# Kernel optimization log

Hardware: AMD Instinct MI355X
Metric: run time of the kernel (lower is better)

The kernel has to match this reference:

```python
import jax, jax.numpy as jnp
import numpy as np

N, P, E = 100000, 10000, 500000
DN, DP, DK, SKIP, MLP_H = 256, 128, 100, 27, 64
E_MEAN, E_STD = 4.0, 2.0
ETA_MEAN, ETA_STD = 0.0, 1.5
ATT_NORM = 0.1  # 1/sqrt(100)
LN_EPS, RMS_EPS = 1e-5, 1e-6


def setup_inputs() -> dict:
    key = jax.random.key(0)
    ks = jax.random.split(key, 32)
    DIN = DN + SKIP  # 283
    s = 0.05
    inp = {
        'node_hidden': jax.random.normal(ks[0], (N, DN), jnp.float32),
        'energy': jax.random.uniform(ks[1], (N,), jnp.float32, 0.01, 1.0),
        'eta': jax.random.normal(ks[2], (N,), jnp.float32),
        'phi': jax.random.normal(ks[3], (N,), jnp.float32),
        'layer': jax.random.uniform(ks[4], (N,), jnp.float32),
        'eta_l': jax.random.normal(ks[5], (N, 6), jnp.float32),
        'phi_l': jax.random.normal(ks[6], (N, 6), jnp.float32),
        'ene_l': jax.random.normal(ks[7], (N, 6), jnp.float32),
        'track_feats': jax.random.uniform(ks[8], (N, 5), jnp.float32),
        'particle_hidden': jax.random.normal(ks[9], (P, DP), jnp.float32),
        'global_rep': jax.random.normal(ks[10], (P, DN), jnp.float32),
        'edge_src': jax.random.randint(ks[11], (E,), 0, N, jnp.int32),
        'edge_dst': jax.random.randint(ks[12], (E,), 0, P, jnp.int32),
        # learned params
        'W_key': jax.random.normal(ks[13], (DIN, DK), jnp.float32) * s,
        'b_key': jnp.zeros((DK,), jnp.float32),
        'W_val': jax.random.normal(ks[14], (DIN, DP), jnp.float32) * s,
        'b_val': jnp.zeros((DP,), jnp.float32),
        'W_q': jax.random.normal(ks[15], (DP + DN, DK), jnp.float32) * s,
        'b_q': jnp.zeros((DK,), jnp.float32),
        'W_ih': jax.random.normal(ks[16], (DP, 3 * DP), jnp.float32) * s,
        'b_ih': jnp.zeros((3 * DP,), jnp.float32),
        'W_hh': jax.random.normal(ks[17], (DP, 3 * DP), jnp.float32) * s,
        'b_hh': jnp.zeros((3 * DP,), jnp.float32),
        'ln_g': jnp.ones((DP,), jnp.float32),
        'ln_b': jnp.zeros((DP,), jnp.float32),
        'W1': jax.random.normal(ks[18], (DP, MLP_H), jnp.float32) * s,
        'b1': jnp.zeros((MLP_H,), jnp.float32),
        'W2': jax.random.normal(ks[19], (MLP_H, DP), jnp.float32) * s,
        'b2': jnp.zeros((DP,), jnp.float32),
        'rms_w': jnp.ones((DP,), jnp.float32),
        'lin_w': jax.random.normal(ks[20], (1, DP), jnp.float32),
    }
    return inp


def _forward(node_hidden, energy, eta, phi, layer, eta_l, phi_l, ene_l, track_feats,
             particle_hidden, global_rep,
             W_key, b_key, W_val, b_val, W_q, b_q, W_ih, b_ih, W_hh, b_hh,
             ln_g, ln_b, W1, b1, W2, b2, rms_w, lin_w, edge_src, edge_dst):
    # --- build node inputs: hidden rep + 27 skip scalars (same order as torch cat) ---
    skip = jnp.concatenate([
        ((jnp.log(energy) - E_MEAN) / E_STD)[:, None],
        ((eta - ETA_MEAN) / ETA_STD)[:, None],
        phi[:, None], layer[:, None],
        (eta_l - ETA_MEAN) / ETA_STD,  # eta_l1..l6
        phi_l, ene_l,
        track_feats,  # isTrack, nTracks, tracks_pt, nTracks_4, tracks_pt_4
    ], axis=1)  # [N, 27]
    x = jnp.concatenate([node_hidden, skip], axis=1)  # [N, 283]
    keys = x @ W_key + b_key      # [N, 100]
    vals = x @ W_val + b_val      # [N, DP]
    q = jnp.concatenate([particle_hidden, global_rep], axis=1) @ W_q + b_q  # [P, 100]

    # --- per-edge attention (note: node_update consumes RAW relu attention) ---
    att = jax.nn.relu(jnp.sum(keys[edge_src] * q[edge_dst], axis=1) * ATT_NORM)  # [E]
    msg = att[:, None] * vals[edge_src]                                          # [E, DP]
    ws = jax.ops.segment_sum(msg, edge_dst, num_segments=P)                      # [P, DP]

    # --- node update: rmsnorm * sigmoid(eltwise) gating, GRU, LN, MLP residual ---
    rms = ws * jax.lax.rsqrt(jnp.mean(ws * ws, axis=-1, keepdims=True) + RMS_EPS) * rms_w
    gated = rms * jax.nn.sigmoid(ws * lin_w)

    h = particle_hidden
    gi = gated @ W_ih + b_ih
    gh = h @ W_hh + b_hh
    i_r, i_z, i_n = jnp.split(gi, 3, axis=1)
    h_r, h_z, h_n = jnp.split(gh, 3, axis=1)
    r = jax.nn.sigmoid(i_r + h_r)
    z = jax.nn.sigmoid(i_z + h_z)
    n = jnp.tanh(i_n + r * h_n)
    h_new = (1.0 - z) * n + z * h

    mu = jnp.mean(h_new, axis=-1, keepdims=True)
    var = jnp.mean((h_new - mu) ** 2, axis=-1, keepdims=True)
    ln = (h_new - mu) * jax.lax.rsqrt(var + LN_EPS) * ln_g + ln_b
    mlp = jax.nn.relu(ln @ W1 + b1) @ W2 + b2
    return h + mlp  # updated particle 'node hidden rep'


def reference(node_hidden, energy, eta, phi, layer, eta_l, phi_l, ene_l, track_feats,
              particle_hidden, global_rep, edge_src, edge_dst,
              W_key, b_key, W_val, b_val, W_q, b_q, W_ih, b_ih, W_hh, b_hh,
              ln_g, ln_b, W1, b1, W2, b2, rms_w, lin_w):
    return _forward(node_hidden, energy, eta, phi, layer, eta_l, phi_l, ene_l, track_feats,
                    particle_hidden, global_rep,
                    W_key, b_key, W_val, b_val, W_q, b_q, W_ih, b_ih, W_hh, b_hh,
                    ln_g, ln_b, W1, b1, W2, b2, rms_w, lin_w, edge_src, edge_dst)
```

## Files before the change

kernel.cpp:

```cpp
#include <hip/hip_runtime.h>
#include <hip/hip_bf16.h>
#include <math.h>

#define THREADS 256

typedef __bf16 bf16_t;
typedef __bf16 bf16x8 __attribute__((ext_vector_type(8)));
typedef float f32x4 __attribute__((ext_vector_type(4)));

__device__ __forceinline__ float sigmoidf_(float x) { return 1.f / (1.f + expf(-x)); }

__device__ __forceinline__ void gload_lds16(const void* g, void* l) {
    __builtin_amdgcn_global_load_lds((const __attribute__((address_space(1))) void*)g,
                                     (__attribute__((address_space(3))) void*)l, 16, 0, 0);
}

__device__ __forceinline__ bf16x8 cvt8(float4 a, float4 b) {
    bf16x8 v;
    v[0] = (bf16_t)a.x; v[1] = (bf16_t)a.y; v[2] = (bf16_t)a.z; v[3] = (bf16_t)a.w;
    v[4] = (bf16_t)b.x; v[5] = (bf16_t)b.y; v[6] = (bf16_t)b.z; v[7] = (bf16_t)b.w;
    return v;
}

__global__ void prep_kernel(const float* __restrict__ W_key, const float* __restrict__ W_val,
                            const float* __restrict__ W_q, const float* __restrict__ b_key,
                            const float* __restrict__ b_val, const float* __restrict__ b_q,
                            bf16_t* __restrict__ WbfT, bf16_t* __restrict__ WqT,
                            float* __restrict__ bpn, float* __restrict__ bpq)
{
    int i = blockIdx.x * THREADS + threadIdx.x;
    const int NW = 256 * 288, NQ = 128 * 384;
    if (i < NW) {
        int c = i / 288, k = i - c * 288;
        float v = 0.f;
        if (k < 283) {
            if (c < 100) v = W_key[k * 100 + c];
            else if (c >= 128 && c < 256) v = W_val[k * 128 + (c - 128)];
        }
        WbfT[i] = (bf16_t)v;
    } else if (i < NW + NQ) {
        int j = i - NW;
        int c = j / 384, k = j - c * 384;
        WqT[j] = (bf16_t)((c < 100) ? W_q[k * 100 + c] : 0.f);
    } else if (i < NW + NQ + 256) {
        int c = i - NW - NQ;
        bpn[c] = (c < 100) ? b_key[c] : ((c >= 128 && c < 256) ? b_val[c - 128] : 0.f);
    } else if (i < NW + NQ + 256 + 128) {
        int c = i - NW - NQ - 256;
        bpq[c] = (c < 100) ? b_q[c] : 0.f;
    }
}

__global__ void prep2_kernel(const float* __restrict__ W_ih, const float* __restrict__ W_hh,
                             const float* __restrict__ b_ih, const float* __restrict__ b_hh,
                             const float* __restrict__ W1, const float* __restrict__ b1,
                             const float* __restrict__ W2,
                             bf16_t* __restrict__ BTg, bf16_t* __restrict__ W1Tp,
                             bf16_t* __restrict__ W2Tp, float* __restrict__ bgru,
                             float* __restrict__ b1p,
                             int* __restrict__ cnt, int twoP,
                             bf16_t* __restrict__ AG, int padStart, int padElems)
{
    int i = blockIdx.x * THREADS + threadIdx.x;
    const int NG = 768 * 256, N1 = 128 * 128, N2 = 128 * 128;
    const int NB = NG + N1 + N2 + 768 + 128;
    if (i < NG) {
        int c = i >> 8, k = i & 255;
        float v = 0.f;
        if (c < 384) { if (k < 128) v = W_ih[k * 384 + c]; }
        else         { if (k >= 128) v = W_hh[(k - 128) * 384 + (c - 384)]; }
        BTg[i] = (bf16_t)v;
    } else if (i < NG + N1) {
        int j = i - NG; int c = j >> 7, k = j & 127;
        W1Tp[j] = (bf16_t)((c < 64) ? W1[k * 64 + c] : 0.f);
    } else if (i < NG + N1 + N2) {
        int j = i - NG - N1; int c = j >> 7, k = j & 127;
        W2Tp[j] = (bf16_t)((k < 64) ? W2[k * 128 + c] : 0.f);
    } else if (i < NG + N1 + N2 + 768) {
        int c = i - NG - N1 - N2;
        bgru[c] = (c < 384) ? b_ih[c] : b_hh[c - 384];
    } else if (i < NB) {
        int c = i - NG - N1 - N2 - 768;
        b1p[c] = (c < 64) ? b1[c] : 0.f;
    } else if (i < NB + twoP) {
        cnt[i - NB] = 0;
    } else if (i < NB + twoP + padElems) {
        int j = i - NB - twoP;
        AG[(size_t)padStart * 256 + j] = (bf16_t)0.f;
    }
}

__global__ void skip_kernel(const float* __restrict__ energy, const float* __restrict__ eta,
                            const float* __restrict__ phi, const float* __restrict__ layer,
                            const float* __restrict__ eta_l, const float* __restrict__ phi_l,
                            const float* __restrict__ ene_l, const float* __restrict__ track,
                            bf16_t* __restrict__ skipb, int N_, int Mpad)
{
    int n = blockIdx.x * THREADS + threadIdx.x;
    if (n >= Mpad) return;
    float o[32];
#pragma unroll
    for (int j = 0; j < 32; ++j) o[j] = 0.f;
    if (n < N_) {
        o[0] = (logf(energy[n]) - 4.0f) * 0.5f;
        o[1] = eta[n] * (1.f / 1.5f);
        o[2] = phi[n];
        o[3] = layer[n];
#pragma unroll
        for (int j = 0; j < 6; ++j) o[4 + j]  = eta_l[n * 6 + j] * (1.f / 1.5f);
#pragma unroll
        for (int j = 0; j < 6; ++j) o[10 + j] = phi_l[n * 6 + j];
#pragma unroll
        for (int j = 0; j < 6; ++j) o[16 + j] = ene_l[n * 6 + j];
#pragma unroll
        for (int j = 0; j < 5; ++j) o[22 + j] = track[n * 5 + j];
    }
    bf16_t* dst = skipb + (size_t)n * 32;
#pragma unroll
    for (int g = 0; g < 4; ++g) {
        bf16x8 v;
#pragma unroll
        for (int j = 0; j < 8; ++j) v[j] = (bf16_t)o[g * 8 + j];
        *(bf16x8*)(dst + g * 8) = v;
    }
}

__global__ __launch_bounds__(256) void kv_gemm(
    const float* __restrict__ nh, const bf16_t* __restrict__ skipb,
    const bf16_t* __restrict__ BT, const float* __restrict__ bias,
    bf16_t* __restrict__ KVb, int N_)
{
    int tid = threadIdx.x;
    int w = tid >> 6, lane = tid & 63;
    int la = lane & 15, hi = lane >> 4;
    int row0 = blockIdx.x * 32;
    int col0 = w * 64;
    int r0 = row0 + la, r1 = row0 + 16 + la;
    bool ok0 = r0 < N_, ok1 = r1 < N_;
    const float* pa0 = nh + (size_t)r0 * 256 + hi * 8;
    const float* pa1 = nh + (size_t)r1 * 256 + hi * 8;

    f32x4 zero4 = {0.f, 0.f, 0.f, 0.f};
    f32x4 acc[2][4];
#pragma unroll
    for (int i = 0; i < 2; ++i)
#pragma unroll
        for (int j = 0; j < 4; ++j) acc[i][j] = zero4;

    for (int kt = 0; kt < 288; kt += 32) {
        bf16x8 a0, a1;
        if (kt < 256) {
            bf16x8 z = {};
            a0 = ok0 ? cvt8(*(const float4*)(pa0 + kt), *(const float4*)(pa0 + kt + 4)) : z;
            a1 = ok1 ? cvt8(*(const float4*)(pa1 + kt), *(const float4*)(pa1 + kt + 4)) : z;
        } else {
            a0 = *(const bf16x8*)(skipb + (size_t)r0 * 32 + hi * 8);
            a1 = *(const bf16x8*)(skipb + (size_t)r1 * 32 + hi * 8);
        }
        bf16x8 b[4];
#pragma unroll
        for (int j = 0; j < 4; ++j)
            b[j] = *(const bf16x8*)(BT + (size_t)(col0 + j * 16 + la) * 288 + kt + hi * 8);
#pragma unroll
        for (int j = 0; j < 4; ++j) {
            acc[0][j] = __builtin_amdgcn_mfma_f32_16x16x32_bf16(a0, b[j], acc[0][j], 0, 0, 0);
            acc[1][j] = __builtin_amdgcn_mfma_f32_16x16x32_bf16(a1, b[j], acc[1][j], 0, 0, 0);
        }
    }

#pragma unroll
    for (int j = 0; j < 4; ++j) {
        int col = col0 + j * 16 + la;
        float bb = bias[col];
#pragma unroll
        for (int i = 0; i < 2; ++i) {
#pragma unroll
            for (int r = 0; r < 4; ++r) {
                int row = row0 + i * 16 + hi * 4 + r;
                KVb[(size_t)row * 256 + col] = (bf16_t)(acc[i][j][r] + bb);
            }
        }
    }
}

template <int MODE>
__global__ __launch_bounds__(256) void mfma_gemm(
    const void* __restrict__ A0, const void* __restrict__ A1,
    const bf16_t* __restrict__ BT, const float* __restrict__ bias,
    void* __restrict__ out0v, const float* __restrict__ resid,
    int K, int Mlimit, int Nrows)
{
    __shared__ short AsS[64 * 32];
    __shared__ short BsS[128 * 32];
    int tid = threadIdx.x;
    int lane = tid & 63, w = tid >> 6;
    int la = lane & 15, hi = lane >> 4;
    int m0 = (w & 1) * 32, n0 = (w >> 1) * 64;
    int row0 = blockIdx.y * 64, col0 = blockIdx.x * 128;

    f32x4 zero4 = {0.f, 0.f, 0.f, 0.f};
    f32x4 acc[2][4];
#pragma unroll
    for (int i = 0; i < 2; ++i)
#pragma unroll
        for (int j = 0; j < 4; ++j) acc[i][j] = zero4;

    const int ra = tid >> 2, ka = (tid & 3) * 8;
    const int c1 = tid + 256;
    const int rb0 = tid >> 2, kb0 = (tid & 3) * 8;
    const int rb1 = c1 >> 2,  kb1 = (c1 & 3) * 8;

    for (int kt = 0; kt < K; kt += 32) {
        int gmA = row0 + ra;
        if (MODE == 1) {
            int gk = kt + ka;
            bf16x8 v = {};
            if (gmA < Nrows) {
                const float* s = (gk < 128) ? ((const float*)A0 + (size_t)gmA * 128 + gk)
                                            : ((const float*)A1 + (size_t)gmA * 256 + (gk - 128));
                v = cvt8(*(const float4*)s, *(const float4*)(s + 4));
            }
            *(bf16x8*)(AsS + (size_t)tid * 8) = v;
        } else {
            gload_lds16((const bf16_t*)A0 + (size_t)gmA * K + kt + ka,
                        AsS + (size_t)tid * 8);
        }
        gload_lds16(BT + (size_t)(col0 + rb0) * K + kt + kb0, BsS + (size_t)tid * 8);
        gload_lds16(BT + (size_t)(col0 + rb1) * K + kt + kb1, BsS + (size_t)c1 * 8);
        __syncthreads();
        bf16x8 a[2], b[4];
#pragma unroll
        for (int i = 0; i < 2; ++i)
            a[i] = *(const bf16x8*)(AsS + (m0 + i * 16 + la) * 32 + hi * 8);
#pragma unroll
        for (int j = 0; j < 4; ++j)
            b[j] = *(const bf16x8*)(BsS + (n0 + j * 16 + la) * 32 + hi * 8);
#pragma unroll
        for (int i = 0; i < 2; ++i)
#pragma unroll
            for (int j = 0; j < 4; ++j)
                acc[i][j] = __builtin_amdgcn_mfma_f32_16x16x32_bf16(a[i], b[j], acc[i][j], 0, 0, 0);
        __syncthreads();
    }

#pragma unroll
    for (int i = 0; i < 2; ++i) {
#pragma unroll
        for (int j = 0; j < 4; ++j) {
            int col = col0 + n0 + j * 16 + la;
            float bb = bias[col];
#pragma unroll
            for (int r = 0; r < 4; ++r) {
                int row = row0 + m0 + i * 16 + hi * 4 + r;
                float v = acc[i][j][r] + bb;
                if (MODE == 1) {
                    ((bf16_t*)out0v)[(size_t)row * 128 + col] = (bf16_t)v;
                } else if (MODE == 2) {
                    ((float*)out0v)[(size_t)row * 768 + col] = v;
                } else if (MODE == 3) {
                    ((bf16_t*)out0v)[(size_t)row * 128 + col] = (bf16_t)fmaxf(v, 0.f);
                } else {
                    if (row < Mlimit)
                        ((float*)out0v)[(size_t)row * 128 + col] = v + resid[(size_t)row * 128 + col];
                }
            }
        }
    }
}

__global__ void hist_kernel(const int* __restrict__ dst, int* __restrict__ cnt, int E_)
{
    int i = blockIdx.x * THREADS + threadIdx.x;
    if (i < E_) atomicAdd(&cnt[dst[i]], 1);
}

__global__ void scan_kernel(const int* __restrict__ cnt, int* __restrict__ offb, int P_)
{
    __shared__ int wsum[16];
    int tid = threadIdx.x;
    int lane = tid & 63, w = tid >> 6;
    int base = tid * 10;
    int c[10];
    int s = 0;
#pragma unroll
    for (int j = 0; j < 10; ++j) {
        int i = base + j;
        c[j] = (i < P_) ? cnt[i] : 0;
        s += c[j];
    }
    int pre = s;
    for (int o = 1; o < 64; o <<= 1) {
        int t = __shfl_up(pre, o);
        if (lane >= o) pre += t;
    }
    if (lane == 63) wsum[w] = pre;
    __syncthreads();
    if (w == 0 && lane < 16) {
        int v = wsum[lane];
        for (int o = 1; o < 16; o <<= 1) {
            int t = __shfl_up(v, o, 16);
            if (lane >= o) v += t;
        }
        wsum[lane] = v;
    }
    __syncthreads();
    int waveoff = (w == 0) ? 0 : wsum[w - 1];
    int run = waveoff + pre - s;
#pragma unroll
    for (int j = 0; j < 10; ++j) {
        int i = base + j;
        if (i <= P_) offb[i] = run;
        run += c[j];
    }
}

__global__ void fill_src_kernel(const int* __restrict__ dst, const int* __restrict__ src,
                                const int* __restrict__ offb, int* __restrict__ cur,
                                int* __restrict__ csrc, int E_)
{
    int i = blockIdx.x * THREADS + threadIdx.x;
    if (i < E_) {
        int d = dst[i];
        int pos = atomicAdd(&cur[d], 1);
        csrc[offb[d] + pos] = src[i];
    }
}

__global__ __launch_bounds__(256) void edge_kernel(
    const int* __restrict__ offb, const int* __restrict__ csrc,
    const bf16_t* __restrict__ KVb, const bf16_t* __restrict__ Qb,
    const float* __restrict__ ph, const float* __restrict__ rms_w,
    const float* __restrict__ lin_w, bf16_t* __restrict__ AG, int P_)
{
    int tid = threadIdx.x;
    int p = blockIdx.x * 4 + (tid >> 6);
    if (p >= P_) return;
    int lane = tid & 63;
    int c = lane & 15, g = lane >> 4;

    bf16x8 q8 = *(const bf16x8*)(Qb + (size_t)p * 128 + c * 8);
    float qf[8];
#pragma unroll
    for (int j = 0; j < 8; ++j) qf[j] = (float)q8[j];

    int s0 = offb[p], e0 = offb[p + 1];
    float acc[8] = {};

    int i = s0 + g;
    for (; i + 12 < e0; i += 16) {
        int n0 = csrc[i], n1 = csrc[i + 4], n2 = csrc[i + 8], n3 = csrc[i + 12];
        const bf16_t* b0 = KVb + (size_t)n0 * 256 + c * 8;
        const bf16_t* b1 = KVb + (size_t)n1 * 256 + c * 8;
        const bf16_t* b2 = KVb + (size_t)n2 * 256 + c * 8;
        const bf16_t* b3 = KVb + (size_t)n3 * 256 + c * 8;
        bf16x8 k0 = *(const bf16x8*)b0, v0 = *(const bf16x8*)(b0 + 128);
        bf16x8 k1 = *(const bf16x8*)b1, v1 = *(const bf16x8*)(b1 + 128);
        bf16x8 k2 = *(const bf16x8*)b2, v2 = *(const bf16x8*)(b2 + 128);
        bf16x8 k3 = *(const bf16x8*)b3, v3 = *(const bf16x8*)(b3 + 128);
        float d0 = 0.f, d1 = 0.f, d2 = 0.f, d3 = 0.f;
#pragma unroll
        for (int j = 0; j < 8; ++j) {
            d0 += qf[j] * (float)k0[j]; d1 += qf[j] * (float)k1[j];
            d2 += qf[j] * (float)k2[j]; d3 += qf[j] * (float)k3[j];
        }
        d0 += __shfl_xor(d0, 1); d1 += __shfl_xor(d1, 1); d2 += __shfl_xor(d2, 1); d3 += __shfl_xor(d3, 1);
        d0 += __shfl_xor(d0, 2); d1 += __shfl_xor(d1, 2); d2 += __shfl_xor(d2, 2); d3 += __shfl_xor(d3, 2);
        d0 += __shfl_xor(d0, 4); d1 += __shfl_xor(d1, 4); d2 += __shfl_xor(d2, 4); d3 += __shfl_xor(d3, 4);
        d0 += __shfl_xor(d0, 8); d1 += __shfl_xor(d1, 8); d2 += __shfl_xor(d2, 8); d3 += __shfl_xor(d3, 8);
        float a0 = fmaxf(d0 * 0.1f, 0.f), a1 = fmaxf(d1 * 0.1f, 0.f);
        float a2 = fmaxf(d2 * 0.1f, 0.f), a3 = fmaxf(d3 * 0.1f, 0.f);
#pragma unroll
        for (int j = 0; j < 8; ++j)
            acc[j] += a0 * (float)v0[j] + a1 * (float)v1[j]
                    + a2 * (float)v2[j] + a3 * (float)v3[j];
    }
    for (; i < e0; i += 4) {
        int nA = csrc[i];
        const bf16_t* bA = KVb + (size_t)nA * 256 + c * 8;
        bf16x8 kA = *(const bf16x8*)bA;
        bf16x8 vA = *(const bf16x8*)(bA + 128);
        float dA = 0.f;
#pragma unroll
        for (int j = 0; j < 8; ++j) dA += qf[j] * (float)kA[j];
        dA += __shfl_xor(dA, 1);
        dA += __shfl_xor(dA, 2);
        dA += __shfl_xor(dA, 4);
        dA += __shfl_xor(dA, 8);
        float aA = fmaxf(dA * 0.1f, 0.f);
#pragma unroll
        for (int j = 0; j < 8; ++j) acc[j] += aA * (float)vA[j];
    }

#pragma unroll
    for (int j = 0; j < 8; ++j) {
        acc[j] += __shfl_xor(acc[j], 16);
        acc[j] += __shfl_xor(acc[j], 32);
    }

    float ss = 0.f;
#pragma unroll
    for (int j = 0; j < 8; ++j) ss += acc[j] * acc[j];
    ss += __shfl_xor(ss, 1); ss += __shfl_xor(ss, 2); ss += __shfl_xor(ss, 4); ss += __shfl_xor(ss, 8);
    float scale = rsqrtf(ss * (1.f / 128.f) + 1e-6f);
    if (g == 0) {
        int cb = c * 8;
        const float* hp = ph + (size_t)p * 128 + cb;
        float4 ha = *(const float4*)hp, hb = *(const float4*)(hp + 4);
        float hv[8] = {ha.x, ha.y, ha.z, ha.w, hb.x, hb.y, hb.z, hb.w};
        bf16x8 gv, hvb;
#pragma unroll
        for (int j = 0; j < 8; ++j) {
            float wsv = acc[j];
            float rv = wsv * scale * rms_w[cb + j];
            gv[j] = (bf16_t)(rv * sigmoidf_(wsv * lin_w[cb + j]));
            hvb[j] = (bf16_t)hv[j];
        }
        *(bf16x8*)(AG + (size_t)p * 256 + cb) = gv;
        *(bf16x8*)(AG + (size_t)p * 256 + 128 + cb) = hvb;
    }
}

__global__ void gru_ln_kernel(const float* __restrict__ G768, const float* __restrict__ ph,
                              const float* __restrict__ ln_g, const float* __restrict__ ln_b,
                              bf16_t* __restrict__ LNb, int P_, int Mq)
{
    int tid = threadIdx.x;
    int g = tid >> 4, s = tid & 15;
    int p = blockIdx.x * 16 + g;
    if (p >= Mq) return;
    int cb = s * 8;
    if (p >= P_) {
        bf16x8 z = {};
        *(bf16x8*)(LNb + (size_t)p * 128 + cb) = z;
        return;
    }
    const float* G = G768 + (size_t)p * 768;
    float ir[8], iz[8], in_[8], hr[8], hz[8], hn_[8], hv[8];
#pragma unroll
    for (int q = 0; q < 2; ++q) {
        float4 v;
        v = *(const float4*)(G + cb + q * 4);        ir[q*4]=v.x; ir[q*4+1]=v.y; ir[q*4+2]=v.z; ir[q*4+3]=v.w;
        v = *(const float4*)(G + 128 + cb + q * 4);  iz[q*4]=v.x; iz[q*4+1]=v.y; iz[q*4+2]=v.z; iz[q*4+3]=v.w;
        v = *(const float4*)(G + 256 + cb + q * 4);  in_[q*4]=v.x; in_[q*4+1]=v.y; in_[q*4+2]=v.z; in_[q*4+3]=v.w;
        v = *(const float4*)(G + 384 + cb + q * 4);  hr[q*4]=v.x; hr[q*4+1]=v.y; hr[q*4+2]=v.z; hr[q*4+3]=v.w;
        v = *(const float4*)(G + 512 + cb + q * 4);  hz[q*4]=v.x; hz[q*4+1]=v.y; hz[q*4+2]=v.z; hz[q*4+3]=v.w;
        v = *(const float4*)(G + 640 + cb + q * 4);  hn_[q*4]=v.x; hn_[q*4+1]=v.y; hn_[q*4+2]=v.z; hn_[q*4+3]=v.w;
        v = *(const float4*)(ph + (size_t)p * 128 + cb + q * 4);
        hv[q*4]=v.x; hv[q*4+1]=v.y; hv[q*4+2]=v.z; hv[q*4+3]=v.w;
    }
    float hn[8];
    float sm = 0.f, sq = 0.f;
#pragma unroll
    for (int j = 0; j < 8; ++j) {
        float r = sigmoidf_(ir[j] + hr[j]);
        float z = sigmoidf_(iz[j] + hz[j]);
        float n = tanhf(in_[j] + r * hn_[j]);
        hn[j] = (1.f - z) * n + z * hv[j];
        sm += hn[j]; sq += hn[j] * hn[j];
    }
    sm += __shfl_xor(sm, 1); sm += __shfl_xor(sm, 2); sm += __shfl_xor(sm, 4); sm += __shfl_xor(sm, 8);
    sq += __shfl_xor(sq, 1); sq += __shfl_xor(sq, 2); sq += __shfl_xor(sq, 4); sq += __shfl_xor(sq, 8);
    float mu = sm * (1.f / 128.f);
    float var = sq * (1.f / 128.f) - mu * mu;
    float iv = rsqrtf(var + 1e-5f);
    bf16x8 o;
#pragma unroll
    for (int j = 0; j < 8; ++j) {
        int c = cb + j;
        o[j] = (bf16_t)((hn[j] - mu) * iv * ln_g[c] + ln_b[c]);
    }
    *(bf16x8*)(LNb + (size_t)p * 128 + cb) = o;
}

extern "C" void kernel_launch(void* const* d_in, const int* in_sizes, int n_in,
                              void* d_out, int out_size, void* d_ws, size_t ws_size,
                              hipStream_t stream)
{
    const float* nh      = (const float*)d_in[0];
    const float* energy  = (const float*)d_in[1];
    const float* eta     = (const float*)d_in[2];
    const float* phi     = (const float*)d_in[3];
    const float* layer   = (const float*)d_in[4];
    const float* eta_l   = (const float*)d_in[5];
    const float* phi_l   = (const float*)d_in[6];
    const float* ene_l   = (const float*)d_in[7];
    const float* track   = (const float*)d_in[8];
    const float* ph      = (const float*)d_in[9];
    const float* grep    = (const float*)d_in[10];
    const int*   esrc    = (const int*)d_in[11];
    const int*   edst    = (const int*)d_in[12];
    const float* W_key   = (const float*)d_in[13];
    const float* b_key   = (const float*)d_in[14];
    const float* W_val   = (const float*)d_in[15];
    const float* b_val   = (const float*)d_in[16];
    const float* W_q     = (const float*)d_in[17];
    const float* b_q     = (const float*)d_in[18];
    const float* W_ih    = (const float*)d_in[19];
    const float* b_ih    = (const float*)d_in[20];
    const float* W_hh    = (const float*)d_in[21];
    const float* b_hh    = (const float*)d_in[22];
    const float* ln_g    = (const float*)d_in[23];
    const float* ln_b    = (const float*)d_in[24];
    const float* W1      = (const float*)d_in[25];
    const float* b1      = (const float*)d_in[26];
    const float* W2      = (const float*)d_in[27];
    const float* b2      = (const float*)d_in[28];
    const float* rms_w   = (const float*)d_in[29];
    const float* lin_w   = (const float*)d_in[30];

    const int N = in_sizes[1];
    const int P = in_sizes[9] / 128;
    const int E = in_sizes[11];
    const int Mpad = ((N + 127) / 128) * 128;
    const int Mq   = ((P + 127) / 128) * 128;

    char* base = (char*)d_ws;
    size_t off = 0;
    auto alloc = [&](size_t bytes) { void* p = base + off; off = (off + bytes + 255) & ~(size_t)255; return p; };
    bf16_t* skipb = (bf16_t*)alloc((size_t)Mpad * 32 * 2);
    bf16_t* WbfT  = (bf16_t*)alloc(256 * 288 * 2);
    bf16_t* WqT   = (bf16_t*)alloc(128 * 384 * 2);
    float*  bpn   = (float*)alloc(256 * 4);
    float*  bpq   = (float*)alloc(128 * 4);
    bf16_t* KVb   = (bf16_t*)alloc((size_t)Mpad * 256 * 2);
    bf16_t* Qb    = (bf16_t*)alloc((size_t)Mq * 128 * 2);
    int*    cnt   = (int*)alloc((size_t)(2 * P) * 4);
    int*    cur   = cnt + P;
    int*    offb  = (int*)alloc((size_t)(P + 1) * 4);
    int*    csrc  = (int*)alloc((size_t)E * 4);
    bf16_t* AG    = (bf16_t*)alloc((size_t)Mq * 256 * 2);
    bf16_t* BTg   = (bf16_t*)alloc(768 * 256 * 2);
    bf16_t* W1Tp  = (bf16_t*)alloc(128 * 128 * 2);
    bf16_t* W2Tp  = (bf16_t*)alloc(128 * 128 * 2);
    float*  bgru  = (float*)alloc(768 * 4);
    float*  b1p   = (float*)alloc(128 * 4);
    float*  G768  = (float*)alloc((size_t)Mq * 768 * 4);
    bf16_t* LNb   = (bf16_t*)alloc((size_t)Mq * 128 * 2);
    bf16_t* M1    = (bf16_t*)alloc((size_t)Mq * 128 * 2);

    {
        int total = 256 * 288 + 128 * 384 + 256 + 128;
        prep_kernel<<<(total + THREADS - 1) / THREADS, THREADS, 0, stream>>>(
            W_key, W_val, W_q, b_key, b_val, b_q, WbfT, WqT, bpn, bpq);
        int padElems = (Mq - P) * 256;
        int total2 = 768 * 256 + 128 * 128 + 128 * 128 + 768 + 128 + 2 * P + padElems;
        prep2_kernel<<<(total2 + THREADS - 1) / THREADS, THREADS, 0, stream>>>(
            W_ih, W_hh, b_ih, b_hh, W1, b1, W2, BTg, W1Tp, W2Tp, bgru, b1p,
            cnt, 2 * P, AG, P, padElems);
        skip_kernel<<<(Mpad + THREADS - 1) / THREADS, THREADS, 0, stream>>>(
            energy, eta, phi, layer, eta_l, phi_l, ene_l, track, skipb, N, Mpad);
    }
    kv_gemm<<<Mpad / 32, THREADS, 0, stream>>>(nh, skipb, WbfT, bpn, KVb, N);
    mfma_gemm<1><<<dim3(1, Mq / 64), THREADS, 0, stream>>>(
        ph, grep, WqT, bpq, Qb, nullptr, 384, 0, P);
    hist_kernel<<<(E + THREADS - 1) / THREADS, THREADS, 0, stream>>>(edst, cnt, E);
    scan_kernel<<<1, 1024, 0, stream>>>(cnt, offb, P);
    fill_src_kernel<<<(E + THREADS - 1) / THREADS, THREADS, 0, stream>>>(
        edst, esrc, offb, cur, csrc, E);
    edge_kernel<<<(P + 3) / 4, THREADS, 0, stream>>>(
        offb, csrc, KVb, Qb, ph, rms_w, lin_w, AG, P);
    mfma_gemm<2><<<dim3(6, Mq / 64), THREADS, 0, stream>>>(
        AG, nullptr, BTg, bgru, G768, nullptr, 256, 0, Mq);
    gru_ln_kernel<<<Mq / 16, THREADS, 0, stream>>>(G768, ph, ln_g, ln_b, LNb, P, Mq);
    mfma_gemm<3><<<dim3(1, Mq / 64), THREADS, 0, stream>>>(
        LNb, nullptr, W1Tp, b1p, M1, nullptr, 128, 0, Mq);
    mfma_gemm<4><<<dim3(1, Mq / 64), THREADS, 0, stream>>>(
        M1, nullptr, W2Tp, b2, d_out, ph, 128, P, Mq);
}
```

Measured before the change: 263.9 us.

## Stage node rows in LDS and double row tile in kv_gemm

The key/value GEMM now loads a 64-row tile of node_hidden plus the skip features into shared memory once per block, converting to bf16 on the way. All four waves then read their A fragments from LDS instead of each re-reading and re-converting from global memory. The row tile grows from 32 to 64, giving 16 accumulators per wave and halving weight reloads per row. The cost is 36KB of LDS, which lowers occupancy, a non-overlapped load phase before the MFMA loop, and possible LDS bank conflicts from the unpadded row stride.

```diff
diff --git a/kernel.cpp b/kernel.cpp
--- a/kernel.cpp
+++ b/kernel.cpp
@@ -6,6 +6,7 @@
 
 typedef __bf16 bf16_t;
 typedef __bf16 bf16x8 __attribute__((ext_vector_type(8)));
+typedef __bf16 bf16x4 __attribute__((ext_vector_type(4)));
 typedef float f32x4 __attribute__((ext_vector_type(4)));
 
 __device__ __forceinline__ float sigmoidf_(float x) { return 1.f / (1.f + expf(-x)); }
@@ -130,42 +131,53 @@
     const bf16_t* __restrict__ BT, const float* __restrict__ bias,
     bf16_t* __restrict__ KVb, int N_)
 {
+    __shared__ short As[64 * 288];
     int tid = threadIdx.x;
     int w = tid >> 6, lane = tid & 63;
     int la = lane & 15, hi = lane >> 4;
-    int row0 = blockIdx.x * 32;
+    int row0 = blockIdx.x * 64;
     int col0 = w * 64;
-    int r0 = row0 + la, r1 = row0 + 16 + la;
-    bool ok0 = r0 < N_, ok1 = r1 < N_;
-    const float* pa0 = nh + (size_t)r0 * 256 + hi * 8;
-    const float* pa1 = nh + (size_t)r1 * 256 + hi * 8;
+
+#pragma unroll
+    for (int r = 0; r < 16; ++r) {
+        int row = r * 4 + w;
+        int grow = row0 + row;
+        float4 f = make_float4(0.f, 0.f, 0.f, 0.f);
+        if (grow < N_) f = *(const float4*)(nh + (size_t)grow * 256 + lane * 4);
+        bf16x4 h;
+        h[0] = (bf16_t)f.x; h[1] = (bf16_t)f.y; h[2] = (bf16_t)f.z; h[3] = (bf16_t)f.w;
+        *(bf16x4*)(As + row * 288 + lane * 4) = h;
+    }
+    {
+        int row = tid >> 2, part = tid & 3;
+        bf16x8 s = *(const bf16x8*)(skipb + (size_t)(row0 + row) * 32 + part * 8);
+        *(bf16x8*)(As + row * 288 + 256 + part * 8) = s;
+    }
+    __syncthreads();
 
     f32x4 zero4 = {0.f, 0.f, 0.f, 0.f};
-    f32x4 acc[2][4];
-#pragma unroll
-    for (int i = 0; i < 2; ++i)
+    f32x4 acc[4][4];
+#pragma unroll
+    for (int i = 0; i < 4; ++i)
 #pragma unroll
         for (int j = 0; j < 4; ++j) acc[i][j] = zero4;
 
-    for (int kt = 0; kt < 288; kt += 32) {
-        bf16x8 a0, a1;
-        if (kt < 256) {
-            bf16x8 z = {};
-            a0 = ok0 ? cvt8(*(const float4*)(pa0 + kt), *(const float4*)(pa0 + kt + 4)) : z;
-            a1 = ok1 ? cvt8(*(const float4*)(pa1 + kt), *(const float4*)(pa1 + kt + 4)) : z;
-        } else {
-            a0 = *(const bf16x8*)(skipb + (size_t)r0 * 32 + hi * 8);
-            a1 = *(const bf16x8*)(skipb + (size_t)r1 * 32 + hi * 8);
-        }
+#pragma unroll
+    for (int t = 0; t < 9; ++t) {
+        int kt = t * 32;
         bf16x8 b[4];
 #pragma unroll
         for (int j = 0; j < 4; ++j)
             b[j] = *(const bf16x8*)(BT + (size_t)(col0 + j * 16 + la) * 288 + kt + hi * 8);
-#pragma unroll
-        for (int j = 0; j < 4; ++j) {
-            acc[0][j] = __builtin_amdgcn_mfma_f32_16x16x32_bf16(a0, b[j], acc[0][j], 0, 0, 0);
-            acc[1][j] = __builtin_amdgcn_mfma_f32_16x16x32_bf16(a1, b[j], acc[1][j], 0, 0, 0);
-        }
+        bf16x8 a[4];
+#pragma unroll
+        for (int i = 0; i < 4; ++i)
+            a[i] = *(const bf16x8*)(As + (i * 16 + la) * 288 + kt + hi * 8);
+#pragma unroll
+        for (int i = 0; i < 4; ++i)
+#pragma unroll
+            for (int j = 0; j < 4; ++j)
+                acc[i][j] = __builtin_amdgcn_mfma_f32_16x16x32_bf16(a[i], b[j], acc[i][j], 0, 0, 0);
     }
 
 #pragma unroll
@@ -173,7 +185,7 @@
         int col = col0 + j * 16 + la;
         float bb = bias[col];
 #pragma unroll
-        for (int i = 0; i < 2; ++i) {
+        for (int i = 0; i < 4; ++i) {
 #pragma unroll
             for (int r = 0; r < 4; ++r) {
                 int row = row0 + i * 16 + hi * 4 + r;
@@ -550,7 +562,7 @@
         skip_kernel<<<(Mpad + THREADS - 1) / THREADS, THREADS, 0, stream>>>(
             energy, eta, phi, layer, eta_l, phi_l, ene_l, track, skipb, N, Mpad);
     }
-    kv_gemm<<<Mpad / 32, THREADS, 0, stream>>>(nh, skipb, WbfT, bpn, KVb, N);
+    kv_gemm<<<Mpad / 64, THREADS, 0, stream>>>(nh, skipb, WbfT, bpn, KVb, N);
     mfma_gemm<1><<<dim3(1, Mq / 64), THREADS, 0, stream>>>(
         ph, grep, WqT, bpq, Qb, nullptr, 384, 0, P);
     hist_kernel<<<(E + THREADS - 1) / THREADS, THREADS, 0, stream>>>(edst, cnt, E);
```

Measured after the change: 226.1 us. 14.3% less time.
